# Optimization experiments

Measured on AMD Instinct MI355X. Metric: run time of the kernel, lower is better.

The kernel has to match this reference:

```python
import jax, jax.numpy as jnp
import numpy as np
import math

N_HEADS = 8
FACTOR = 1


def setup_inputs() -> dict:
    key = jax.random.key(0)
    k1, k2, k3 = jax.random.split(key, 3)
    B, L, E = 16, 2048, 512
    return {
        "queries": jax.random.normal(k1, (B, L, E), dtype=jnp.float32),
        "keys": jax.random.normal(k2, (B, L, E), dtype=jnp.float32),
        "values": jax.random.normal(k3, (B, L, E), dtype=jnp.float32),
        "attn_mask": jnp.zeros((1,), dtype=bool),  # unused by the original forward
    }


def _time_delay_agg(values, corr, factor):
    # values, corr: (B, H, L, C)
    B, H, L, C = values.shape
    top_k = max(1, int(factor * math.log(L)))
    # NOTE: topk over the last (channel) axis, faithfully matching the source.
    weights, delay = jax.lax.top_k(corr, top_k)          # (B,H,L,K)
    weights = jax.nn.softmax(weights, axis=-1)
    positions = jnp.arange(L).reshape(1, 1, L, 1)
    delay_idx = (positions - delay) % L                   # (B,H,L,K), time indices
    idx = delay_idx.reshape(B, H, L * top_k, 1)
    gathered = jnp.take_along_axis(values, idx, axis=2)   # (B,H,L*K,C)
    gathered = gathered.reshape(B, H, L, top_k, C)
    return (gathered * weights[..., None]).sum(axis=3)    # (B,H,L,C)


def reference(queries, keys, values, attn_mask):
    B, L, E = queries.shape
    _, S, _ = values.shape
    H = N_HEADS
    hd = E // H
    q = queries.reshape(B, L, H, hd).transpose(0, 2, 1, 3)  # (B,H,L,hd)
    k = keys.reshape(B, S, H, hd).transpose(0, 2, 1, 3)
    v = values.reshape(B, S, H, hd).transpose(0, 2, 1, 3)
    if L > S:
        pad = L - S
        zeros = jnp.zeros((B, H, pad, hd), dtype=v.dtype)
        v = jnp.concatenate([v, zeros], axis=2)
        k = jnp.concatenate([k, zeros], axis=2)
    else:
        v = v[:, :, :L, :]
        k = k[:, :, :L, :]
    # period-based dependency discovery via FFT cross-correlation along time
    q_fft = jnp.fft.rfft(q, axis=2)
    k_fft = jnp.fft.rfft(k, axis=2)
    corr = jnp.fft.irfft(q_fft * jnp.conj(k_fft), n=L, axis=2)  # (B,H,L,hd)
    out = _time_delay_agg(v, corr, FACTOR)                       # (B,H,L,hd)
    return out.transpose(0, 2, 1, 3).reshape(B, L, E)
```

## Files before the change

### kernel.cpp

```cpp
#include <hip/hip_runtime.h>
#include <math.h>

#define LEN   2048
#define EDIM  512
#define NB    16
#define NH    8
#define HD    64
#define TOPK  7
#define LDSN  (LEN + (LEN >> 5))

__device__ inline float2 cmul(float2 a, float2 b) {
    return make_float2(a.x * b.x - a.y * b.y, a.x * b.y + a.y * b.x);
}
__device__ inline float2 cadd(float2 a, float2 b) { return make_float2(a.x + b.x, a.y + b.y); }
__device__ inline float2 csub(float2 a, float2 b) { return make_float2(a.x - b.x, a.y - b.y); }
__device__ inline int pidx(int i) { return i + (i >> 5); }

__global__ __launch_bounds__(256) void transpose_qk(const float* __restrict__ q,
                                                    const float* __restrict__ k,
                                                    float* __restrict__ qT,
                                                    float* __restrict__ kT) {
    __shared__ float tile[32][33];
    int b  = blockIdx.z;
    int e0 = blockIdx.x * 32;
    int t0 = blockIdx.y * 32;
    const float* qb = q + (size_t)b * LEN * EDIM;
    const float* kb = k + (size_t)b * LEN * EDIM;
    float* qTb = qT + (size_t)b * EDIM * LEN;
    float* kTb = kT + (size_t)b * EDIM * LEN;
    int x = threadIdx.x;
    int y = threadIdx.y;
    for (int r = 0; r < 32; r += 8)
        tile[y + r][x] = qb[(size_t)(t0 + y + r) * EDIM + e0 + x];
    __syncthreads();
    for (int r = 0; r < 32; r += 8)
        qTb[(size_t)(e0 + y + r) * LEN + t0 + x] = tile[x][y + r];
    __syncthreads();
    for (int r = 0; r < 32; r += 8)
        tile[y + r][x] = kb[(size_t)(t0 + y + r) * EDIM + e0 + x];
    __syncthreads();
    for (int r = 0; r < 32; r += 8)
        kTb[(size_t)(e0 + y + r) * LEN + t0 + x] = tile[x][y + r];
}

__device__ inline void tw8(float ang, float2* w) {
    float s, c;
    sincosf(ang, &s, &c);
    w[1] = make_float2(c, s);
    w[2] = cmul(w[1], w[1]);
    w[3] = cmul(w[2], w[1]);
    w[4] = cmul(w[2], w[2]);
    w[5] = cmul(w[3], w[2]);
    w[6] = cmul(w[3], w[3]);
    w[7] = cmul(w[4], w[3]);
}

__device__ inline void fwd8(float2* P, int base, int stride, const float2* w) {
    const float C = 0.70710678118654752f;
    float2 v[8];
    #pragma unroll
    for (int r = 0; r < 8; ++r) v[r] = P[pidx(base + stride * r)];
    float2 y0 = cadd(v[0], v[4]), y1 = cadd(v[1], v[5]);
    float2 y2 = cadd(v[2], v[6]), y3 = cadd(v[3], v[7]);
    float2 t0 = csub(v[0], v[4]), t1 = csub(v[1], v[5]);
    float2 t2 = csub(v[2], v[6]), t3 = csub(v[3], v[7]);
    float2 z0 = t0;
    float2 z1 = make_float2(C * (t1.x + t1.y), C * (t1.y - t1.x));
    float2 z2 = make_float2(t2.y, -t2.x);
    float2 z3 = make_float2(C * (t3.y - t3.x), -C * (t3.x + t3.y));
    float2 a0 = cadd(y0, y2), a1 = cadd(y1, y3);
    float2 b0 = csub(y0, y2), tb = csub(y1, y3);
    float2 b1 = make_float2(tb.y, -tb.x);
    float2 c0 = cadd(z0, z2), c1 = cadd(z1, z3);
    float2 d0 = csub(z0, z2), td = csub(z1, z3);
    float2 d1 = make_float2(td.y, -td.x);
    float2 X0 = cadd(a0, a1), X4 = csub(a0, a1);
    float2 X2 = cadd(b0, b1), X6 = csub(b0, b1);
    float2 X1 = cadd(c0, c1), X5 = csub(c0, c1);
    float2 X3 = cadd(d0, d1), X7 = csub(d0, d1);
    P[pidx(base)]              = X0;
    P[pidx(base + stride)]     = cmul(X1, w[1]);
    P[pidx(base + 2 * stride)] = cmul(X2, w[2]);
    P[pidx(base + 3 * stride)] = cmul(X3, w[3]);
    P[pidx(base + 4 * stride)] = cmul(X4, w[4]);
    P[pidx(base + 5 * stride)] = cmul(X5, w[5]);
    P[pidx(base + 6 * stride)] = cmul(X6, w[6]);
    P[pidx(base + 7 * stride)] = cmul(X7, w[7]);
}

__device__ inline void inv8(float2* P, int base, int stride, const float2* w) {
    const float C = 0.70710678118654752f;
    float2 v[8];
    #pragma unroll
    for (int p = 0; p < 8; ++p) v[p] = P[pidx(base + stride * p)];
    #pragma unroll
    for (int p = 1; p < 8; ++p) v[p] = cmul(v[p], w[p]);
    float2 y0 = cadd(v[0], v[4]), y1 = cadd(v[1], v[5]);
    float2 y2 = cadd(v[2], v[6]), y3 = cadd(v[3], v[7]);
    float2 t0 = csub(v[0], v[4]), t1 = csub(v[1], v[5]);
    float2 t2 = csub(v[2], v[6]), t3 = csub(v[3], v[7]);
    float2 z0 = t0;
    float2 z1 = make_float2(C * (t1.x - t1.y), C * (t1.x + t1.y));
    float2 z2 = make_float2(-t2.y, t2.x);
    float2 z3 = make_float2(-C * (t3.x + t3.y), C * (t3.x - t3.y));
    float2 a0 = cadd(y0, y2), a1 = cadd(y1, y3);
    float2 b0 = csub(y0, y2), tb = csub(y1, y3);
    float2 b1 = make_float2(-tb.y, tb.x);
    float2 c0 = cadd(z0, z2), c1 = cadd(z1, z3);
    float2 d0 = csub(z0, z2), td = csub(z1, z3);
    float2 d1 = make_float2(-td.y, td.x);
    float2 X0 = cadd(a0, a1), X4 = csub(a0, a1);
    float2 X2 = cadd(b0, b1), X6 = csub(b0, b1);
    float2 X1 = cadd(c0, c1), X5 = csub(c0, c1);
    float2 X3 = cadd(d0, d1), X7 = csub(d0, d1);
    P[pidx(base)]              = X0;
    P[pidx(base + stride)]     = X1;
    P[pidx(base + 2 * stride)] = X2;
    P[pidx(base + 3 * stride)] = X3;
    P[pidx(base + 4 * stride)] = X4;
    P[pidx(base + 5 * stride)] = X5;
    P[pidx(base + 6 * stride)] = X6;
    P[pidx(base + 7 * stride)] = X7;
}

__device__ inline void fwd4(float2* P, int base) {
    int ib = pidx(base);
    float2 v0 = P[ib], v1 = P[ib + 1], v2 = P[ib + 2], v3 = P[ib + 3];
    float2 a0 = cadd(v0, v2), a1 = cadd(v1, v3);
    float2 b0 = csub(v0, v2), t = csub(v1, v3);
    float2 b1 = make_float2(t.y, -t.x);
    P[ib]     = cadd(a0, a1);
    P[ib + 2] = csub(a0, a1);
    P[ib + 1] = cadd(b0, b1);
    P[ib + 3] = csub(b0, b1);
}
__device__ inline void inv4(float2* P, int base) {
    int ib = pidx(base);
    float2 v0 = P[ib], v1 = P[ib + 1], v2 = P[ib + 2], v3 = P[ib + 3];
    float2 a0 = cadd(v0, v2), a1 = cadd(v1, v3);
    float2 b0 = csub(v0, v2), t = csub(v1, v3);
    float2 b1 = make_float2(-t.y, t.x);
    P[ib]     = cadd(a0, a1);
    P[ib + 2] = csub(a0, a1);
    P[ib + 1] = cadd(b0, b1);
    P[ib + 3] = csub(b0, b1);
}

__device__ inline int slotOf(int k) {
    return ((k & 7) << 8) | (((k >> 3) & 7) << 5) | (((k >> 6) & 7) << 2) | ((k >> 9) & 3);
}

__device__ inline void fft_core(float2* A, float2* Bs, int tid) {
    const float PI2 = 6.283185307179586f;
    float2 w[8];
    tw8(-PI2 * (float)tid * (1.0f / 2048.0f), w);
    fwd8(A, tid, 256, w);
    fwd8(Bs, tid, 256, w);
    __syncthreads();
    {
        int c = tid >> 5, q = tid & 31, base = c * 256 + q;
        tw8(-PI2 * (float)q * (1.0f / 256.0f), w);
        fwd8(A, base, 32, w);
        fwd8(Bs, base, 32, w);
    }
    __syncthreads();
    {
        int c = tid >> 2, q = tid & 3, base = c * 32 + q;
        tw8(-PI2 * (float)q * (1.0f / 32.0f), w);
        fwd8(A, base, 4, w);
        fwd8(Bs, base, 4, w);
    }
    __syncthreads();
    fwd4(A, 4 * tid);  fwd4(A, 4 * (tid + 256));
    fwd4(Bs, 4 * tid); fwd4(Bs, 4 * (tid + 256));
    __syncthreads();
    for (int f = tid; f <= 1024; f += 256) {
        int nf = (2048 - f) & 2047;
        int ia = pidx(slotOf(f));
        int ib = pidx(slotOf(nf));
        float2 z1 = A[ia],  z1n = A[ib];
        float2 z2 = Bs[ia], z2n = Bs[ib];
        float Qx = 0.5f * (z1.x + z1n.x), Qy = 0.5f * (z1.y - z1n.y);
        float Kx = 0.5f * (z1.y + z1n.y), Ky = 0.5f * (z1n.x - z1.x);
        float C1x = Qx * Kx + Qy * Ky;
        float C1y = Qy * Kx - Qx * Ky;
        float Px = 0.5f * (z2.x + z2n.x), Py = 0.5f * (z2.y - z2n.y);
        float Lx = 0.5f * (z2.y + z2n.y), Ly = 0.5f * (z2n.x - z2.x);
        float C2x = Px * Lx + Py * Ly;
        float C2y = Py * Lx - Px * Ly;
        A[ia] = make_float2(C1x - C2y, C1y + C2x);
        if (f != 0 && f != 1024)
            A[ib] = make_float2(C1x + C2y, C2x - C1y);
    }
    __syncthreads();
    inv4(A, 4 * tid); inv4(A, 4 * (tid + 256));
    __syncthreads();
    {
        int c = tid >> 2, q = tid & 3, base = c * 32 + q;
        tw8(PI2 * (float)q * (1.0f / 32.0f), w);
        inv8(A, base, 4, w);
    }
    __syncthreads();
    {
        int c = tid >> 5, q = tid & 31, base = c * 256 + q;
        tw8(PI2 * (float)q * (1.0f / 256.0f), w);
        inv8(A, base, 32, w);
    }
    __syncthreads();
    tw8(PI2 * (float)tid * (1.0f / 2048.0f), w);
    inv8(A, tid, 256, w);
    __syncthreads();
}

__global__ __launch_bounds__(256) void fft_corr(const float* qT,
                                                const float* kT,
                                                float* corr) {
    __shared__ float2 A[LDSN];
    __shared__ float2 Bs[LDSN];
    int ch0 = blockIdx.x * 2;
    int tid = threadIdx.x;
    const float4* q4 = (const float4*)(qT + (size_t)ch0 * LEN);
    const float4* k4 = (const float4*)(kT + (size_t)ch0 * LEN);
    for (int t4 = tid; t4 < LEN / 4; t4 += 256) {
        float4 qa = q4[t4],           ka = k4[t4];
        float4 qb = q4[t4 + LEN / 4], kb = k4[t4 + LEN / 4];
        int t  = t4 * 4;
        int ib = t + (t >> 5);
        A[ib]      = make_float2(qa.x, ka.x);
        A[ib + 1]  = make_float2(qa.y, ka.y);
        A[ib + 2]  = make_float2(qa.z, ka.z);
        A[ib + 3]  = make_float2(qa.w, ka.w);
        Bs[ib]     = make_float2(qb.x, kb.x);
        Bs[ib + 1] = make_float2(qb.y, kb.y);
        Bs[ib + 2] = make_float2(qb.z, kb.z);
        Bs[ib + 3] = make_float2(qb.w, kb.w);
    }
    __syncthreads();
    fft_core(A, Bs, tid);
    const float inv = 1.0f / (float)LEN;
    float4* c0 = (float4*)(corr + (size_t)ch0 * LEN);
    float4* c1 = (float4*)(corr + (size_t)(ch0 + 1) * LEN);
    for (int t4 = tid; t4 < LEN / 4; t4 += 256) {
        int t  = t4 * 4;
        int ib = t + (t >> 5);
        c0[t4] = make_float4(A[ib].x * inv, A[ib + 1].x * inv,
                             A[ib + 2].x * inv, A[ib + 3].x * inv);
        c1[t4] = make_float4(A[ib].y * inv, A[ib + 1].y * inv,
                             A[ib + 2].y * inv, A[ib + 3].y * inv);
    }
}

__global__ __launch_bounds__(256) void fft_corr_strided(const float* q,
                                                        const float* k,
                                                        float* corr,
                                                        int chStart) {
    __shared__ float2 A[LDSN];
    __shared__ float2 Bs[LDSN];
    int chLocal = blockIdx.x * 2;
    int gch = chStart + chLocal;
    int b   = gch >> 9;
    int e   = gch & (EDIM - 1);
    int tid = threadIdx.x;
    const float* qr = q + (size_t)b * LEN * EDIM + e;
    const float* kr = k + (size_t)b * LEN * EDIM + e;
    for (int t = tid; t < LEN; t += 256) {
        float2 qv = *(const float2*)(qr + (size_t)t * EDIM);
        float2 kv = *(const float2*)(kr + (size_t)t * EDIM);
        int ib = t + (t >> 5);
        A[ib]  = make_float2(qv.x, kv.x);
        Bs[ib] = make_float2(qv.y, kv.y);
    }
    __syncthreads();
    fft_core(A, Bs, tid);
    const float inv = 1.0f / (float)LEN;
    float4* c0 = (float4*)(corr + (size_t)chLocal * LEN);
    float4* c1 = (float4*)(corr + (size_t)(chLocal + 1) * LEN);
    for (int t4 = tid; t4 < LEN / 4; t4 += 256) {
        int t  = t4 * 4;
        int ib = t + (t >> 5);
        c0[t4] = make_float4(A[ib].x * inv, A[ib + 1].x * inv,
                             A[ib + 2].x * inv, A[ib + 3].x * inv);
        c1[t4] = make_float4(A[ib].y * inv, A[ib + 1].y * inv,
                             A[ib + 2].y * inv, A[ib + 3].y * inv);
    }
}

__global__ __launch_bounds__(256) void topk_agg(const float* __restrict__ corr,
                                                const float* __restrict__ values,
                                                float* __restrict__ out,
                                                int bhBase) {
    __shared__ float2 w_d[256][TOPK];
    int l0 = blockIdx.x * 256;
    int lh = blockIdx.y;
    int bh = bhBase + lh;
    int b  = bh >> 3;
    int h  = bh & 7;
    int tid = threadIdx.x;

    const float* cb = corr + (size_t)lh * HD * LEN + l0 + tid;
    float wk[TOPK];
    int   dk[TOPK];
    #pragma unroll
    for (int t = 0; t < TOPK; ++t) { wk[t] = -INFINITY; dk[t] = 0; }
    #pragma unroll 8
    for (int c = 0; c < HD; ++c) {
        float nv = cb[(size_t)c * LEN];
        int   nd = c;
        #pragma unroll
        for (int t = 0; t < TOPK; ++t) {
            bool  m  = nv > wk[t];
            float tv = wk[t]; int td = dk[t];
            wk[t] = m ? nv : tv;
            dk[t] = m ? nd : td;
            nv    = m ? tv : nv;
            nd    = m ? td : nd;
        }
    }
    float mx = wk[0], sum = 0.f;
    float e[TOPK];
    #pragma unroll
    for (int t = 0; t < TOPK; ++t) { e[t] = expf(wk[t] - mx); sum += e[t]; }
    float invs = 1.f / sum;
    #pragma unroll
    for (int t = 0; t < TOPK; ++t)
        w_d[tid][t] = make_float2(e[t] * invs, __int_as_float(dk[t]));
    __syncthreads();

    int lane = tid & 63;
    int wave = tid >> 6;
    const float* vb = values + (size_t)b * LEN * EDIM + h * HD + lane;
    float*       ob = out    + (size_t)b * LEN * EDIM + h * HD + lane;
    for (int i = 0; i < 64; ++i) {
        int lp = wave * 64 + i;
        int l  = l0 + lp;
        float acc = 0.f;
        #pragma unroll
        for (int t = 0; t < TOPK; ++t) {
            float2 wd = w_d[lp][t];
            int idx = (l - __float_as_int(wd.y)) & (LEN - 1);
            acc += wd.x * vb[(size_t)idx * EDIM];
        }
        ob[(size_t)l * EDIM] = acc;
    }
}

extern "C" void kernel_launch(void* const* d_in, const int* in_sizes, int n_in,
                              void* d_out, int out_size, void* d_ws, size_t ws_size,
                              hipStream_t stream) {
    const float* q = (const float*)d_in[0];
    const float* k = (const float*)d_in[1];
    const float* v = (const float*)d_in[2];
    float* out = (float*)d_out;

    const size_t CORR_BYTES = (size_t)NB * EDIM * LEN * sizeof(float);

    if (ws_size >= CORR_BYTES) {
        float* qT   = (float*)d_ws;
        float* kT   = (float*)d_out;
        float* corr = qT;
        transpose_qk<<<dim3(EDIM / 32, LEN / 32, NB), dim3(32, 8), 0, stream>>>(q, k, qT, kT);
        fft_corr<<<dim3(NB * EDIM / 2), dim3(256), 0, stream>>>(qT, kT, corr);
        topk_agg<<<dim3(LEN / 256, NB * NH), dim3(256), 0, stream>>>(corr, v, out, 0);
    } else {
        const size_t HEAD_BYTES = (size_t)HD * LEN * sizeof(float);
        int headsPer = (int)(ws_size / HEAD_BYTES);
        if (headsPer < 1) headsPer = 1;
        if (headsPer > NB * NH) headsPer = NB * NH;
        float* corr = (float*)d_ws;
        for (int hs = 0; hs < NB * NH; hs += headsPer) {
            int hc = NB * NH - hs < headsPer ? NB * NH - hs : headsPer;
            fft_corr_strided<<<dim3(hc * HD / 2), dim3(256), 0, stream>>>(q, k, corr, hs * HD);
            topk_agg<<<dim3(LEN / 256, hc), dim3(256), 0, stream>>>(corr, v, out, hs);
        }
    }
}
```

Baseline: 342.0 us.

## Vectorize transpose, XOR-swizzle FFT LDS, stage values tile in LDS for aggregation

The transpose kernel moves to 64x64 tiles with float4 global loads and stores. The FFT shared buffers switch from padded indexing to an XOR swizzle, which shrinks LDS per block, and the kernel gets occupancy hints. The top-k aggregation now works on 128-row blocks and preloads a 192-row window of values into LDS, so the delayed gathers read shared memory instead of scattered global memory. The LDS gather relies on delays being below 64, which holds because delays are channel indices, and it costs an extra halo load per block.

Result: slower. 369.7 us (+8.1%).

```diff
diff --git a/kernel.cpp b/kernel.cpp
--- a/kernel.cpp
+++ b/kernel.cpp
@@ -7,40 +7,67 @@
 #define NH    8
 #define HD    64
 #define TOPK  7
-#define LDSN  (LEN + (LEN >> 5))
+#define LBLK  128
+#define VROWS (LBLK + 64)
 
 __device__ inline float2 cmul(float2 a, float2 b) {
     return make_float2(a.x * b.x - a.y * b.y, a.x * b.y + a.y * b.x);
 }
 __device__ inline float2 cadd(float2 a, float2 b) { return make_float2(a.x + b.x, a.y + b.y); }
 __device__ inline float2 csub(float2 a, float2 b) { return make_float2(a.x - b.x, a.y - b.y); }
-__device__ inline int pidx(int i) { return i + (i >> 5); }
+__device__ inline int sw(int i) { return i ^ ((i >> 5) & 15); }
 
 __global__ __launch_bounds__(256) void transpose_qk(const float* __restrict__ q,
                                                     const float* __restrict__ k,
                                                     float* __restrict__ qT,
                                                     float* __restrict__ kT) {
-    __shared__ float tile[32][33];
+    __shared__ float tile[64][65];
     int b  = blockIdx.z;
-    int e0 = blockIdx.x * 32;
-    int t0 = blockIdx.y * 32;
+    int e0 = blockIdx.x * 64;
+    int t0 = blockIdx.y * 64;
+    int tid = threadIdx.x;
+    int tr = tid >> 4, cx = tid & 15;
+    int er = tid >> 2, tg = tid & 3;
     const float* qb = q + (size_t)b * LEN * EDIM;
     const float* kb = k + (size_t)b * LEN * EDIM;
     float* qTb = qT + (size_t)b * EDIM * LEN;
     float* kTb = kT + (size_t)b * EDIM * LEN;
-    int x = threadIdx.x;
-    int y = threadIdx.y;
-    for (int r = 0; r < 32; r += 8)
-        tile[y + r][x] = qb[(size_t)(t0 + y + r) * EDIM + e0 + x];
-    __syncthreads();
-    for (int r = 0; r < 32; r += 8)
-        qTb[(size_t)(e0 + y + r) * LEN + t0 + x] = tile[x][y + r];
-    __syncthreads();
-    for (int r = 0; r < 32; r += 8)
-        tile[y + r][x] = kb[(size_t)(t0 + y + r) * EDIM + e0 + x];
-    __syncthreads();
-    for (int r = 0; r < 32; r += 8)
-        kTb[(size_t)(e0 + y + r) * LEN + t0 + x] = tile[x][y + r];
+
+    #pragma unroll
+    for (int i = 0; i < 4; ++i) {
+        int row = tr + 16 * i;
+        float4 v = *(const float4*)(qb + (size_t)(t0 + row) * EDIM + e0 + 4 * cx);
+        tile[4 * cx + 0][row] = v.x;
+        tile[4 * cx + 1][row] = v.y;
+        tile[4 * cx + 2][row] = v.z;
+        tile[4 * cx + 3][row] = v.w;
+    }
+    __syncthreads();
+    #pragma unroll
+    for (int i = 0; i < 4; ++i) {
+        int seg = tg + 4 * i;
+        float4 v = make_float4(tile[er][4 * seg + 0], tile[er][4 * seg + 1],
+                               tile[er][4 * seg + 2], tile[er][4 * seg + 3]);
+        *(float4*)(qTb + (size_t)(e0 + er) * LEN + t0 + 4 * seg) = v;
+    }
+    __syncthreads();
+    #pragma unroll
+    for (int i = 0; i < 4; ++i) {
+        int row = tr + 16 * i;
+        float4 v = *(const float4*)(kb + (size_t)(t0 + row) * EDIM + e0 + 4 * cx);
+        tile[4 * cx + 0][row] = v.x;
+        tile[4 * cx + 1][row] = v.y;
+        tile[4 * cx + 2][row] = v.z;
+        tile[4 * cx + 3][row] = v.w;
+    }
+    __syncthreads();
+    #pragma unroll
+    for (int i = 0; i < 4; ++i) {
+        int seg = tg + 4 * i;
+        float4 v = make_float4(tile[er][4 * seg + 0], tile[er][4 * seg + 1],
+                               tile[er][4 * seg + 2], tile[er][4 * seg + 3]);
+        *(float4*)(kTb + (size_t)(e0 + er) * LEN + t0 + 4 * seg) = v;
+    }
 }
 
 __device__ inline void tw8(float ang, float2* w) {
@@ -59,7 +86,7 @@
     const float C = 0.70710678118654752f;
     float2 v[8];
     #pragma unroll
-    for (int r = 0; r < 8; ++r) v[r] = P[pidx(base + stride * r)];
+    for (int r = 0; r < 8; ++r) v[r] = P[sw(base + stride * r)];
     float2 y0 = cadd(v[0], v[4]), y1 = cadd(v[1], v[5]);
     float2 y2 = cadd(v[2], v[6]), y3 = cadd(v[3], v[7]);
     float2 t0 = csub(v[0], v[4]), t1 = csub(v[1], v[5]);
@@ -78,21 +105,21 @@
     float2 X2 = cadd(b0, b1), X6 = csub(b0, b1);
     float2 X1 = cadd(c0, c1), X5 = csub(c0, c1);
     float2 X3 = cadd(d0, d1), X7 = csub(d0, d1);
-    P[pidx(base)]              = X0;
-    P[pidx(base + stride)]     = cmul(X1, w[1]);
-    P[pidx(base + 2 * stride)] = cmul(X2, w[2]);
-    P[pidx(base + 3 * stride)] = cmul(X3, w[3]);
-    P[pidx(base + 4 * stride)] = cmul(X4, w[4]);
-    P[pidx(base + 5 * stride)] = cmul(X5, w[5]);
-    P[pidx(base + 6 * stride)] = cmul(X6, w[6]);
-    P[pidx(base + 7 * stride)] = cmul(X7, w[7]);
+    P[sw(base)]              = X0;
+    P[sw(base + stride)]     = cmul(X1, w[1]);
+    P[sw(base + 2 * stride)] = cmul(X2, w[2]);
+    P[sw(base + 3 * stride)] = cmul(X3, w[3]);
+    P[sw(base + 4 * stride)] = cmul(X4, w[4]);
+    P[sw(base + 5 * stride)] = cmul(X5, w[5]);
+    P[sw(base + 6 * stride)] = cmul(X6, w[6]);
+    P[sw(base + 7 * stride)] = cmul(X7, w[7]);
 }
 
 __device__ inline void inv8(float2* P, int base, int stride, const float2* w) {
     const float C = 0.70710678118654752f;
     float2 v[8];
     #pragma unroll
-    for (int p = 0; p < 8; ++p) v[p] = P[pidx(base + stride * p)];
+    for (int p = 0; p < 8; ++p) v[p] = P[sw(base + stride * p)];
     #pragma unroll
     for (int p = 1; p < 8; ++p) v[p] = cmul(v[p], w[p]);
     float2 y0 = cadd(v[0], v[4]), y1 = cadd(v[1], v[5]);
@@ -113,37 +140,35 @@
     float2 X2 = cadd(b0, b1), X6 = csub(b0, b1);
     float2 X1 = cadd(c0, c1), X5 = csub(c0, c1);
     float2 X3 = cadd(d0, d1), X7 = csub(d0, d1);
-    P[pidx(base)]              = X0;
-    P[pidx(base + stride)]     = X1;
-    P[pidx(base + 2 * stride)] = X2;
-    P[pidx(base + 3 * stride)] = X3;
-    P[pidx(base + 4 * stride)] = X4;
-    P[pidx(base + 5 * stride)] = X5;
-    P[pidx(base + 6 * stride)] = X6;
-    P[pidx(base + 7 * stride)] = X7;
+    P[sw(base)]              = X0;
+    P[sw(base + stride)]     = X1;
+    P[sw(base + 2 * stride)] = X2;
+    P[sw(base + 3 * stride)] = X3;
+    P[sw(base + 4 * stride)] = X4;
+    P[sw(base + 5 * stride)] = X5;
+    P[sw(base + 6 * stride)] = X6;
+    P[sw(base + 7 * stride)] = X7;
 }
 
 __device__ inline void fwd4(float2* P, int base) {
-    int ib = pidx(base);
-    float2 v0 = P[ib], v1 = P[ib + 1], v2 = P[ib + 2], v3 = P[ib + 3];
+    float2 v0 = P[sw(base)], v1 = P[sw(base + 1)], v2 = P[sw(base + 2)], v3 = P[sw(base + 3)];
     float2 a0 = cadd(v0, v2), a1 = cadd(v1, v3);
     float2 b0 = csub(v0, v2), t = csub(v1, v3);
     float2 b1 = make_float2(t.y, -t.x);
-    P[ib]     = cadd(a0, a1);
-    P[ib + 2] = csub(a0, a1);
-    P[ib + 1] = cadd(b0, b1);
-    P[ib + 3] = csub(b0, b1);
+    P[sw(base)]     = cadd(a0, a1);
+    P[sw(base + 2)] = csub(a0, a1);
+    P[sw(base + 1)] = cadd(b0, b1);
+    P[sw(base + 3)] = csub(b0, b1);
 }
 __device__ inline void inv4(float2* P, int base) {
-    int ib = pidx(base);
-    float2 v0 = P[ib], v1 = P[ib + 1], v2 = P[ib + 2], v3 = P[ib + 3];
+    float2 v0 = P[sw(base)], v1 = P[sw(base + 1)], v2 = P[sw(base + 2)], v3 = P[sw(base + 3)];
     float2 a0 = cadd(v0, v2), a1 = cadd(v1, v3);
     float2 b0 = csub(v0, v2), t = csub(v1, v3);
     float2 b1 = make_float2(-t.y, t.x);
-    P[ib]     = cadd(a0, a1);
-    P[ib + 2] = csub(a0, a1);
-    P[ib + 1] = cadd(b0, b1);
-    P[ib + 3] = csub(b0, b1);
+    P[sw(base)]     = cadd(a0, a1);
+    P[sw(base + 2)] = csub(a0, a1);
+    P[sw(base + 1)] = cadd(b0, b1);
+    P[sw(base + 3)] = csub(b0, b1);
 }
 
 __device__ inline int slotOf(int k) {
@@ -176,8 +201,8 @@
     __syncthreads();
     for (int f = tid; f <= 1024; f += 256) {
         int nf = (2048 - f) & 2047;
-        int ia = pidx(slotOf(f));
-        int ib = pidx(slotOf(nf));
+        int ia = sw(slotOf(f));
+        int ib = sw(slotOf(nf));
         float2 z1 = A[ia],  z1n = A[ib];
         float2 z2 = Bs[ia], z2n = Bs[ib];
         float Qx = 0.5f * (z1.x + z1n.x), Qy = 0.5f * (z1.y - z1n.y);
@@ -212,11 +237,11 @@
     __syncthreads();
 }
 
-__global__ __launch_bounds__(256) void fft_corr(const float* qT,
-                                                const float* kT,
-                                                float* corr) {
-    __shared__ float2 A[LDSN];
-    __shared__ float2 Bs[LDSN];
+__global__ __launch_bounds__(256, 5) void fft_corr(const float* qT,
+                                                   const float* kT,
+                                                   float* corr) {
+    __shared__ float2 A[LEN];
+    __shared__ float2 Bs[LEN];
     int ch0 = blockIdx.x * 2;
     int tid = threadIdx.x;
     const float4* q4 = (const float4*)(qT + (size_t)ch0 * LEN);
@@ -224,16 +249,15 @@
     for (int t4 = tid; t4 < LEN / 4; t4 += 256) {
         float4 qa = q4[t4],           ka = k4[t4];
         float4 qb = q4[t4 + LEN / 4], kb = k4[t4 + LEN / 4];
-        int t  = t4 * 4;
-        int ib = t + (t >> 5);
-        A[ib]      = make_float2(qa.x, ka.x);
-        A[ib + 1]  = make_float2(qa.y, ka.y);
-        A[ib + 2]  = make_float2(qa.z, ka.z);
-        A[ib + 3]  = make_float2(qa.w, ka.w);
-        Bs[ib]     = make_float2(qb.x, kb.x);
-        Bs[ib + 1] = make_float2(qb.y, kb.y);
-        Bs[ib + 2] = make_float2(qb.z, kb.z);
-        Bs[ib + 3] = make_float2(qb.w, kb.w);
+        int t = t4 * 4;
+        A[sw(t)]      = make_float2(qa.x, ka.x);
+        A[sw(t + 1)]  = make_float2(qa.y, ka.y);
+        A[sw(t + 2)]  = make_float2(qa.z, ka.z);
+        A[sw(t + 3)]  = make_float2(qa.w, ka.w);
+        Bs[sw(t)]     = make_float2(qb.x, kb.x);
+        Bs[sw(t + 1)] = make_float2(qb.y, kb.y);
+        Bs[sw(t + 2)] = make_float2(qb.z, kb.z);
+        Bs[sw(t + 3)] = make_float2(qb.w, kb.w);
     }
     __syncthreads();
     fft_core(A, Bs, tid);
@@ -241,21 +265,19 @@
     float4* c0 = (float4*)(corr + (size_t)ch0 * LEN);
     float4* c1 = (float4*)(corr + (size_t)(ch0 + 1) * LEN);
     for (int t4 = tid; t4 < LEN / 4; t4 += 256) {
-        int t  = t4 * 4;
-        int ib = t + (t >> 5);
-        c0[t4] = make_float4(A[ib].x * inv, A[ib + 1].x * inv,
-                             A[ib + 2].x * inv, A[ib + 3].x * inv);
-        c1[t4] = make_float4(A[ib].y * inv, A[ib + 1].y * inv,
-                             A[ib + 2].y * inv, A[ib + 3].y * inv);
-    }
-}
-
-__global__ __launch_bounds__(256) void fft_corr_strided(const float* q,
-                                                        const float* k,
-                                                        float* corr,
-                                                        int chStart) {
-    __shared__ float2 A[LDSN];
-    __shared__ float2 Bs[LDSN];
+        int t = t4 * 4;
+        float2 e0 = A[sw(t)], e1 = A[sw(t + 1)], e2 = A[sw(t + 2)], e3 = A[sw(t + 3)];
+        c0[t4] = make_float4(e0.x * inv, e1.x * inv, e2.x * inv, e3.x * inv);
+        c1[t4] = make_float4(e0.y * inv, e1.y * inv, e2.y * inv, e3.y * inv);
+    }
+}
+
+__global__ __launch_bounds__(256, 5) void fft_corr_strided(const float* q,
+                                                           const float* k,
+                                                           float* corr,
+                                                           int chStart) {
+    __shared__ float2 A[LEN];
+    __shared__ float2 Bs[LEN];
     int chLocal = blockIdx.x * 2;
     int gch = chStart + chLocal;
     int b   = gch >> 9;
@@ -266,9 +288,8 @@
     for (int t = tid; t < LEN; t += 256) {
         float2 qv = *(const float2*)(qr + (size_t)t * EDIM);
         float2 kv = *(const float2*)(kr + (size_t)t * EDIM);
-        int ib = t + (t >> 5);
-        A[ib]  = make_float2(qv.x, kv.x);
-        Bs[ib] = make_float2(qv.y, kv.y);
+        A[sw(t)]  = make_float2(qv.x, kv.x);
+        Bs[sw(t)] = make_float2(qv.y, kv.y);
     }
     __syncthreads();
     fft_core(A, Bs, tid);
@@ -276,69 +297,78 @@
     float4* c0 = (float4*)(corr + (size_t)chLocal * LEN);
     float4* c1 = (float4*)(corr + (size_t)(chLocal + 1) * LEN);
     for (int t4 = tid; t4 < LEN / 4; t4 += 256) {
-        int t  = t4 * 4;
-        int ib = t + (t >> 5);
-        c0[t4] = make_float4(A[ib].x * inv, A[ib + 1].x * inv,
-                             A[ib + 2].x * inv, A[ib + 3].x * inv);
-        c1[t4] = make_float4(A[ib].y * inv, A[ib + 1].y * inv,
-                             A[ib + 2].y * inv, A[ib + 3].y * inv);
-    }
-}
-
-__global__ __launch_bounds__(256) void topk_agg(const float* __restrict__ corr,
-                                                const float* __restrict__ values,
-                                                float* __restrict__ out,
-                                                int bhBase) {
-    __shared__ float2 w_d[256][TOPK];
-    int l0 = blockIdx.x * 256;
+        int t = t4 * 4;
+        float2 e0 = A[sw(t)], e1 = A[sw(t + 1)], e2 = A[sw(t + 2)], e3 = A[sw(t + 3)];
+        c0[t4] = make_float4(e0.x * inv, e1.x * inv, e2.x * inv, e3.x * inv);
+        c1[t4] = make_float4(e0.y * inv, e1.y * inv, e2.y * inv, e3.y * inv);
+    }
+}
+
+__global__ __launch_bounds__(256, 2) void topk_agg(const float* __restrict__ corr,
+                                                   const float* __restrict__ values,
+                                                   float* __restrict__ out,
+                                                   int bhBase) {
+    __shared__ float  vtile[VROWS][HD];
+    __shared__ float2 w_d[LBLK][TOPK];
+    int l0 = blockIdx.x * LBLK;
     int lh = blockIdx.y;
     int bh = bhBase + lh;
     int b  = bh >> 3;
     int h  = bh & 7;
     int tid = threadIdx.x;
-
-    const float* cb = corr + (size_t)lh * HD * LEN + l0 + tid;
-    float wk[TOPK];
-    int   dk[TOPK];
-    #pragma unroll
-    for (int t = 0; t < TOPK; ++t) { wk[t] = -INFINITY; dk[t] = 0; }
-    #pragma unroll 8
-    for (int c = 0; c < HD; ++c) {
-        float nv = cb[(size_t)c * LEN];
-        int   nd = c;
+    const float* vb0 = values + (size_t)b * LEN * EDIM + h * HD;
+
+    for (int idx = tid; idx < VROWS * (HD / 4); idx += 256) {
+        int r  = idx >> 4;
+        int c4 = idx & 15;
+        int gr = (l0 - 64 + r) & (LEN - 1);
+        float4 v = *(const float4*)(vb0 + (size_t)gr * EDIM + 4 * c4);
+        *(float4*)&vtile[r][4 * c4] = v;
+    }
+
+    if (tid < LBLK) {
+        const float* cb = corr + (size_t)lh * HD * LEN + l0 + tid;
+        float wk[TOPK];
+        int   dk[TOPK];
         #pragma unroll
-        for (int t = 0; t < TOPK; ++t) {
-            bool  m  = nv > wk[t];
-            float tv = wk[t]; int td = dk[t];
-            wk[t] = m ? nv : tv;
-            dk[t] = m ? nd : td;
-            nv    = m ? tv : nv;
-            nd    = m ? td : nd;
+        for (int t = 0; t < TOPK; ++t) { wk[t] = -INFINITY; dk[t] = 0; }
+        #pragma unroll 8
+        for (int c = 0; c < HD; ++c) {
+            float nv = cb[(size_t)c * LEN];
+            int   nd = c;
+            #pragma unroll
+            for (int t = 0; t < TOPK; ++t) {
+                bool  m  = nv > wk[t];
+                float tv = wk[t]; int td = dk[t];
+                wk[t] = m ? nv : tv;
+                dk[t] = m ? nd : td;
+                nv    = m ? tv : nv;
+                nd    = m ? td : nd;
+            }
         }
-    }
-    float mx = wk[0], sum = 0.f;
-    float e[TOPK];
-    #pragma unroll
-    for (int t = 0; t < TOPK; ++t) { e[t] = expf(wk[t] - mx); sum += e[t]; }
-    float invs = 1.f / sum;
-    #pragma unroll
-    for (int t = 0; t < TOPK; ++t)
-        w_d[tid][t] = make_float2(e[t] * invs, __int_as_float(dk[t]));
+        float mx = wk[0], sum = 0.f;
+        float e[TOPK];
+        #pragma unroll
+        for (int t = 0; t < TOPK; ++t) { e[t] = expf(wk[t] - mx); sum += e[t]; }
+        float invs = 1.f / sum;
+        #pragma unroll
+        for (int t = 0; t < TOPK; ++t)
+            w_d[tid][t] = make_float2(e[t] * invs, __int_as_float(dk[t]));
+    }
     __syncthreads();
 
     int lane = tid & 63;
     int wave = tid >> 6;
-    const float* vb = values + (size_t)b * LEN * EDIM + h * HD + lane;
-    float*       ob = out    + (size_t)b * LEN * EDIM + h * HD + lane;
-    for (int i = 0; i < 64; ++i) {
-        int lp = wave * 64 + i;
+    float* ob = out + (size_t)b * LEN * EDIM + h * HD + lane;
+    for (int i = 0; i < LBLK / 4; ++i) {
+        int lp = wave * (LBLK / 4) + i;
         int l  = l0 + lp;
         float acc = 0.f;
         #pragma unroll
         for (int t = 0; t < TOPK; ++t) {
             float2 wd = w_d[lp][t];
-            int idx = (l - __float_as_int(wd.y)) & (LEN - 1);
-            acc += wd.x * vb[(size_t)idx * EDIM];
+            int r = lp - __float_as_int(wd.y) + 64;
+            acc += wd.x * vtile[r][lane];
         }
         ob[(size_t)l * EDIM] = acc;
     }
@@ -358,9 +388,9 @@
         float* qT   = (float*)d_ws;
         float* kT   = (float*)d_out;
         float* corr = qT;
-        transpose_qk<<<dim3(EDIM / 32, LEN / 32, NB), dim3(32, 8), 0, stream>>>(q, k, qT, kT);
+        transpose_qk<<<dim3(EDIM / 64, LEN / 64, NB), dim3(256), 0, stream>>>(q, k, qT, kT);
         fft_corr<<<dim3(NB * EDIM / 2), dim3(256), 0, stream>>>(qT, kT, corr);
-        topk_agg<<<dim3(LEN / 256, NB * NH), dim3(256), 0, stream>>>(corr, v, out, 0);
+        topk_agg<<<dim3(LEN / LBLK, NB * NH), dim3(256), 0, stream>>>(corr, v, out, 0);
     } else {
         const size_t HEAD_BYTES = (size_t)HD * LEN * sizeof(float);
         int headsPer = (int)(ws_size / HEAD_BYTES);
@@ -370,7 +400,7 @@
         for (int hs = 0; hs < NB * NH; hs += headsPer) {
             int hc = NB * NH - hs < headsPer ? NB * NH - hs : headsPer;
             fft_corr_strided<<<dim3(hc * HD / 2), dim3(256), 0, stream>>>(q, k, corr, hs * HD);
-            topk_agg<<<dim3(LEN / 256, hc), dim3(256), 0, stream>>>(corr, v, out, hs);
+            topk_agg<<<dim3(LEN / LBLK, hc), dim3(256), 0, stream>>>(corr, v, out, hs);
         }
     }
 }
```
